# Kernel optimization log

Hardware: AMD Instinct MI355X
Metric: run time of the kernel (lower is better)

Reference implementation:

```python
import jax, jax.numpy as jnp
import numpy as np

B, T, D, H, E = 2, 1024, 1024, 4096, 8


def setup_inputs() -> dict:
    key = jax.random.key(0)
    ks = jax.random.split(key, 6)
    x = jax.random.normal(ks[0], (B, T, D), dtype=jnp.float32)
    padding_mask = jnp.zeros((B, T), dtype=bool)
    # Gate: Linear(D, E, bias=False) -> weight (E, D)
    Wg = jax.random.normal(ks[1], (E, D), dtype=jnp.float32) * (1.0 / np.sqrt(D))
    # Stacked expert FFN params (torch Linear layout: weight (out, in))
    W1 = jax.random.normal(ks[2], (E, H, D), dtype=jnp.float32) * (1.0 / np.sqrt(D))
    b1 = jax.random.normal(ks[3], (E, H), dtype=jnp.float32) * 0.01
    W2 = jax.random.normal(ks[4], (E, D, H), dtype=jnp.float32) * (1.0 / np.sqrt(H))
    b2 = jax.random.normal(ks[5], (E, D), dtype=jnp.float32) * 0.01
    return {"x": x, "padding_mask": padding_mask, "Wg": Wg, "W1": W1, "b1": b1, "W2": W2, "b2": b2}


def _top2_gate(xt, pm, Wg):
    # xt: (nt, D) flattened tokens, pm: (nt,) bool padding mask
    nt, ec = xt.shape[0], Wg.shape[0]
    logits = (xt @ Wg.T).astype(jnp.float32)            # use_fp32=True
    gate_value = jax.nn.softmax(logits, axis=-1)        # (nt, E)
    gate_value = jnp.where(pm[:, None], 0.0, gate_value)
    top2_idx = jax.lax.top_k(gate_value, 2)[1]          # (nt, 2)
    keep = jax.nn.one_hot(top2_idx, ec, dtype=bool).any(axis=1)  # (nt, E) True at top1/top2
    gate_weights = jnp.where(keep, gate_value, 0.0)
    s = gate_weights.sum(axis=1, keepdims=True)
    s = jnp.where(s == 0.0, 1.0, s)
    gate_weights = gate_weights / s
    # load-balance loss: fraction of top-1 assignments vs mean gate prob per expert
    nt_real = (~pm).sum().astype(jnp.float32)
    top1_counts = (jax.nn.one_hot(top2_idx[:, 0], ec, dtype=jnp.float32)
                   * (~pm)[:, None].astype(jnp.float32)).sum(axis=0)  # (E,)
    lb_loss = ec * ((top1_counts / nt_real) * (gate_value.sum(axis=0) / nt_real)).sum()
    return lb_loss, gate_weights, gate_value


def reference(x, padding_mask, Wg, W1, b1, W2, b2):
    Bx, Tx, Dx = x.shape
    xt = x.reshape(-1, Dx)                   # (nt, D)
    pm = padding_mask.reshape(-1)            # (nt,)
    lb_loss, gw, gate_value = _top2_gate(xt, pm, Wg)
    gw = gw.astype(x.dtype)                  # (nt, E)
    # Expert FFNs (dense over experts; routing weights are zero except top-2)
    h = jax.nn.relu(jnp.einsum('nd,ehd->neh', xt, W1) + b1)   # (nt, E, H)
    y = jnp.einsum('neh,edh->ned', h, W2) + b2                # (nt, E, D)
    out = jnp.einsum('ne,ned->nd', gw, y).reshape(Bx, Tx, Dx)
    return out, gate_value, lb_loss
```

## Files before the change

### kernel.cpp

```cpp
#include <hip/hip_runtime.h>
#include <hip/hip_bf16.h>
#include <stdint.h>


#define NTOK 2048
#define DDIM 1024
#define HDIM 4096
#define NEXP 8
#define KSPLIT 4

typedef float  f32x4  __attribute__((ext_vector_type(4)));
typedef __bf16 bf16x8 __attribute__((ext_vector_type(8)));
typedef __bf16 bf16x4 __attribute__((ext_vector_type(4)));

typedef const __attribute__((address_space(1))) void g1_t;
typedef __attribute__((address_space(3))) void l3_t;
__device__ __forceinline__ void gld16(const void* g, void* l) {
  __builtin_amdgcn_global_load_lds((g1_t*)g, (l3_t*)l, 16, 0, 0);
}

__global__ void init_kernel(int* fill) {
  int t = threadIdx.x;
  if (t < NEXP) fill[t] = 0;
}

__global__ __launch_bounds__(256)
void conv_kernel(const float* __restrict__ src, __bf16* __restrict__ dst, long n8) {
  long i = (long)blockIdx.x * 256 + threadIdx.x;
  long stride = (long)gridDim.x * 256;
  for (; i < n8; i += stride) {
    f32x4 a = ((const f32x4*)src)[2 * i];
    f32x4 b = ((const f32x4*)src)[2 * i + 1];
    bf16x8 o;
#pragma unroll
    for (int q = 0; q < 4; ++q) { o[q] = (__bf16)a[q]; o[q + 4] = (__bf16)b[q]; }
    ((bf16x8*)dst)[i] = o;
  }
}

__global__ __launch_bounds__(256)
void zero_y_kernel(float* __restrict__ y) {
  size_t i = (size_t)blockIdx.x * 256 + threadIdx.x;
  ((f32x4*)y)[i] = (f32x4){0.f, 0.f, 0.f, 0.f};
}

__global__ __launch_bounds__(256)
void gate_kernel(const float* __restrict__ x, const unsigned char* __restrict__ pmask,
                 const float* __restrict__ Wg, float* __restrict__ gate_out,
                 int* __restrict__ tix, float* __restrict__ twt,
                 __bf16* __restrict__ xbf)
{
  int wave = threadIdx.x >> 6, lane = threadIdx.x & 63;
  int t = blockIdx.x * 4 + wave;
  const f32x4* x4 = (const f32x4*)(x + (size_t)t * DDIM);
  const f32x4* w4 = (const f32x4*)Wg;
  bf16x4* xb4 = (bf16x4*)(xbf + (size_t)t * DDIM);
  float acc[NEXP];
#pragma unroll
  for (int e = 0; e < NEXP; ++e) acc[e] = 0.f;
#pragma unroll
  for (int i = 0; i < 4; ++i) {
    f32x4 xv = x4[i * 64 + lane];
    bf16x4 xo;
#pragma unroll
    for (int q = 0; q < 4; ++q) xo[q] = (__bf16)xv[q];
    xb4[i * 64 + lane] = xo;
#pragma unroll
    for (int e = 0; e < NEXP; ++e) {
      f32x4 wv = w4[e * 256 + i * 64 + lane];
      acc[e] += xv[0]*wv[0] + xv[1]*wv[1] + xv[2]*wv[2] + xv[3]*wv[3];
    }
  }
#pragma unroll
  for (int e = 0; e < NEXP; ++e) {
    float v = acc[e];
#pragma unroll
    for (int off = 32; off > 0; off >>= 1) v += __shfl_xor(v, off, 64);
    acc[e] = v;
  }
  if (lane == 0) {
    bool pm = pmask[t] != 0;
    float m = acc[0];
#pragma unroll
    for (int e = 1; e < NEXP; ++e) m = fmaxf(m, acc[e]);
    float g[NEXP]; float s = 0.f;
#pragma unroll
    for (int e = 0; e < NEXP; ++e) { g[e] = expf(acc[e] - m); s += g[e]; }
    float inv = 1.f / s;
#pragma unroll
    for (int e = 0; e < NEXP; ++e) g[e] *= inv;
    if (pm) {
#pragma unroll
      for (int e = 0; e < NEXP; ++e) g[e] = 0.f;
    }
    int i1 = 0;
#pragma unroll
    for (int e = 1; e < NEXP; ++e) if (g[e] > g[i1]) i1 = e;
    int i2 = -1;
#pragma unroll
    for (int e = 0; e < NEXP; ++e) if (e != i1 && (i2 < 0 || g[e] > g[i2])) i2 = e;
    float w1 = g[i1], w2 = g[i2], ss = w1 + w2;
    if (ss == 0.f) ss = 1.f;
    w1 /= ss; w2 /= ss;
#pragma unroll
    for (int e = 0; e < NEXP; ++e) gate_out[(size_t)t * NEXP + e] = g[e];
    tix[2*t] = i1; tix[2*t+1] = i2;
    twt[2*t] = w1; twt[2*t+1] = w2;
  }
}

__global__ __launch_bounds__(1024)
void stats_kernel(const float* __restrict__ gate_out, const int* __restrict__ tix,
                  const unsigned char* __restrict__ pmask,
                  int* __restrict__ ecount, int* __restrict__ offs,
                  float* __restrict__ lb_out)
{
  int tid = threadIdx.x, lane = tid & 63, wv = tid >> 6;
  float lg[NEXP]; float lt1[NEXP]; int lec[NEXP]; float ln = 0.f;
#pragma unroll
  for (int e = 0; e < NEXP; ++e) { lg[e] = 0.f; lt1[e] = 0.f; lec[e] = 0; }
#pragma unroll
  for (int it = 0; it < NTOK / 1024; ++it) {
    int t = tid + it * 1024;
    f32x4 g0 = ((const f32x4*)(gate_out + (size_t)t * NEXP))[0];
    f32x4 g1 = ((const f32x4*)(gate_out + (size_t)t * NEXP))[1];
    lg[0] += g0[0]; lg[1] += g0[1]; lg[2] += g0[2]; lg[3] += g0[3];
    lg[4] += g1[0]; lg[5] += g1[1]; lg[6] += g1[2]; lg[7] += g1[3];
    if (!pmask[t]) {
      int i1 = tix[2*t], i2 = tix[2*t+1];
      lt1[i1] += 1.f; lec[i1] += 1; lec[i2] += 1; ln += 1.f;
    }
  }
#pragma unroll
  for (int e = 0; e < NEXP; ++e) {
#pragma unroll
    for (int off = 32; off > 0; off >>= 1) {
      lg[e]  += __shfl_xor(lg[e],  off, 64);
      lt1[e] += __shfl_xor(lt1[e], off, 64);
      lec[e] += __shfl_xor(lec[e], off, 64);
    }
  }
#pragma unroll
  for (int off = 32; off > 0; off >>= 1) ln += __shfl_xor(ln, off, 64);
  __shared__ float sg[16][NEXP], st[16][NEXP], sn[16];
  __shared__ int   se[16][NEXP];
  if (lane == 0) {
#pragma unroll
    for (int e = 0; e < NEXP; ++e) { sg[wv][e] = lg[e]; st[wv][e] = lt1[e]; se[wv][e] = lec[e]; }
    sn[wv] = ln;
  }
  __syncthreads();
  if (tid == 0) {
    float G[NEXP] = {0}, T1[NEXP] = {0}; int EC[NEXP] = {0}; float N = 0.f;
    for (int w = 0; w < 16; ++w) {
      N += sn[w];
#pragma unroll
      for (int e = 0; e < NEXP; ++e) { G[e] += sg[w][e]; T1[e] += st[w][e]; EC[e] += se[w][e]; }
    }
    int o = 0;
    for (int e = 0; e < NEXP; ++e) { ecount[e] = EC[e]; offs[e] = o; o += EC[e]; }
    if (N <= 0.f) N = 1.f;
    float lb = 0.f;
    for (int e = 0; e < NEXP; ++e) lb += (T1[e] / N) * (G[e] / N);
    lb_out[0] = (float)NEXP * lb;
  }
}

__global__ __launch_bounds__(256)
void compact_kernel(const unsigned char* __restrict__ pmask, const int* __restrict__ tix,
                    const int* __restrict__ offs, int* __restrict__ fill,
                    int* __restrict__ tok_list, int* __restrict__ slot_of)
{
  int t = blockIdx.x * 256 + threadIdx.x;
  int lane = threadIdx.x & 63;
  bool pm = pmask[t] != 0;
#pragma unroll
  for (int j = 0; j < 2; ++j) {
    int e = pm ? -1 : tix[2*t + j];
    int pos = -1;
#pragma unroll
    for (int ex = 0; ex < NEXP; ++ex) {
      unsigned long long mask = __ballot(e == ex);
      if (mask) {
        int leader = (int)(__ffsll((long long)mask) - 1);
        int base = 0;
        if (lane == leader) base = atomicAdd(&fill[ex], (int)__popcll(mask));
        base = __shfl(base, leader, 64);
        if (e == ex)
          pos = offs[ex] + base + (int)__popcll(mask & ((1ull << lane) - 1ull));
      }
    }
    if (e >= 0) { tok_list[pos] = t; slot_of[2*t + j] = pos; }
    else slot_of[2*t + j] = -1;
  }
}

__global__ __launch_bounds__(256)
void gemm1_kernel(const __bf16* __restrict__ xbf, const __bf16* __restrict__ w1bf,
                  const float* __restrict__ b1, const int* __restrict__ ecount,
                  const int* __restrict__ offs, const int* __restrict__ tok_list,
                  __bf16* __restrict__ hbuf)
{
  const int NTILE = HDIM / 128;
  const int MTILE = NTOK / 128;
  int bid = blockIdx.x;
  int e = bid / (MTILE * NTILE);
  int rem = bid % (MTILE * NTILE);
  int mt = rem / NTILE, nt = rem % NTILE;
  int cnt = ecount[e];
  if (mt * 128 >= cnt) return;
  int off = offs[e];

  __shared__ __bf16 At[128 * 64];
  __shared__ __bf16 Bt[128 * 64];

  int tid = threadIdx.x, lane = tid & 63, wave = tid >> 6;
  int wm = wave >> 1, wn = wave & 1;

  const __bf16* aP[4];
  const __bf16* bP[4];
#pragma unroll
  for (int r = 0; r < 4; ++r) {
    int row = r * 32 + wave * 8 + (lane >> 3);
    int mrow = mt * 128 + row;
    int tok = tok_list[off + ((mrow < cnt) ? mrow : 0)];
    aP[r] = xbf + (size_t)tok * DDIM + (lane & 7) * 8;
    bP[r] = w1bf + (size_t)e * HDIM * DDIM + (size_t)(nt * 128 + row) * DDIM + (lane & 7) * 8;
  }
  __bf16* lA = At + wave * 512;
  __bf16* lB = Bt + wave * 512;

  f32x4 acc[4][4];
#pragma unroll
  for (int m = 0; m < 4; ++m)
#pragma unroll
    for (int n = 0; n < 4; ++n) acc[m][n] = (f32x4){0.f, 0.f, 0.f, 0.f};

  for (int k0 = 0; k0 < DDIM; k0 += 64) {
#pragma unroll
    for (int r = 0; r < 4; ++r) {
      gld16(aP[r] + k0, lA + r * 2048);
      gld16(bP[r] + k0, lB + r * 2048);
    }
    __syncthreads();
#pragma unroll
    for (int ks = 0; ks < 2; ++ks) {
      int koff = ks * 32 + (lane >> 4) * 8;
      bf16x8 af[4], bfr[4];
#pragma unroll
      for (int m = 0; m < 4; ++m) af[m] = *(const bf16x8*)&At[(wm*64 + m*16 + (lane & 15)) * 64 + koff];
#pragma unroll
      for (int n = 0; n < 4; ++n) bfr[n] = *(const bf16x8*)&Bt[(wn*64 + n*16 + (lane & 15)) * 64 + koff];
#pragma unroll
      for (int m = 0; m < 4; ++m)
#pragma unroll
        for (int n = 0; n < 4; ++n)
          acc[m][n] = __builtin_amdgcn_mfma_f32_16x16x32_bf16(af[m], bfr[n], acc[m][n], 0, 0, 0);
    }
    __syncthreads();
  }
#pragma unroll
  for (int n = 0; n < 4; ++n) {
    int col = nt * 128 + wn * 64 + n * 16 + (lane & 15);
    float bias = b1[e * HDIM + col];
#pragma unroll
    for (int m = 0; m < 4; ++m) {
#pragma unroll
      for (int j = 0; j < 4; ++j) {
        int mr = mt * 128 + wm * 64 + m * 16 + ((lane >> 4) << 2) + j;
        if (mr < cnt) {
          float v = fmaxf(acc[m][n][j] + bias, 0.f);
          hbuf[(size_t)(off + mr) * HDIM + col] = (__bf16)v;
        }
      }
    }
  }
}

__global__ __launch_bounds__(256)
void gemm2_kernel(const __bf16* __restrict__ hbuf, const __bf16* __restrict__ w2bf,
                  const int* __restrict__ ecount, const int* __restrict__ offs,
                  float* __restrict__ ybuf)
{
  const int NTILE = DDIM / 128;
  const int MTILE = NTOK / 128;
  int bid = blockIdx.x;
  int e = bid / (MTILE * NTILE * KSPLIT);
  int rem = bid % (MTILE * NTILE * KSPLIT);
  int mt = rem / (NTILE * KSPLIT);
  int rem2 = rem % (NTILE * KSPLIT);
  int nt = rem2 / KSPLIT, kc = rem2 % KSPLIT;
  int cnt = ecount[e];
  if (mt * 128 >= cnt) return;
  int off = offs[e];

  __shared__ __bf16 At[128 * 64];
  __shared__ __bf16 Bt[128 * 64];

  int tid = threadIdx.x, lane = tid & 63, wave = tid >> 6;
  int wm = wave >> 1, wn = wave & 1;

  const __bf16* aP[4];
  const __bf16* bP[4];
#pragma unroll
  for (int r = 0; r < 4; ++r) {
    int row = r * 32 + wave * 8 + (lane >> 3);
    aP[r] = hbuf + (size_t)(off + mt * 128 + row) * HDIM + (lane & 7) * 8;
    bP[r] = w2bf + (size_t)e * DDIM * HDIM + (size_t)(nt * 128 + row) * HDIM + (lane & 7) * 8;
  }
  __bf16* lA = At + wave * 512;
  __bf16* lB = Bt + wave * 512;

  f32x4 acc[4][4];
#pragma unroll
  for (int m = 0; m < 4; ++m)
#pragma unroll
    for (int n = 0; n < 4; ++n) acc[m][n] = (f32x4){0.f, 0.f, 0.f, 0.f};

  int kbeg = kc * (HDIM / KSPLIT);
  int kend = kbeg + (HDIM / KSPLIT);
  for (int k0 = kbeg; k0 < kend; k0 += 64) {
#pragma unroll
    for (int r = 0; r < 4; ++r) {
      gld16(aP[r] + k0, lA + r * 2048);
      gld16(bP[r] + k0, lB + r * 2048);
    }
    __syncthreads();
#pragma unroll
    for (int ks = 0; ks < 2; ++ks) {
      int koff = ks * 32 + (lane >> 4) * 8;
      bf16x8 af[4], bfr[4];
#pragma unroll
      for (int m = 0; m < 4; ++m) af[m] = *(const bf16x8*)&At[(wm*64 + m*16 + (lane & 15)) * 64 + koff];
#pragma unroll
      for (int n = 0; n < 4; ++n) bfr[n] = *(const bf16x8*)&Bt[(wn*64 + n*16 + (lane & 15)) * 64 + koff];
#pragma unroll
      for (int m = 0; m < 4; ++m)
#pragma unroll
        for (int n = 0; n < 4; ++n)
          acc[m][n] = __builtin_amdgcn_mfma_f32_16x16x32_bf16(af[m], bfr[n], acc[m][n], 0, 0, 0);
    }
    __syncthreads();
  }
#pragma unroll
  for (int m = 0; m < 4; ++m) {
#pragma unroll
    for (int j = 0; j < 4; ++j) {
      int mr = mt * 128 + wm * 64 + m * 16 + ((lane >> 4) << 2) + j;
      if (mr >= cnt) continue;
      int slot = off + mr;
#pragma unroll
      for (int n = 0; n < 4; ++n) {
        int col = nt * 128 + wn * 64 + n * 16 + (lane & 15);
        atomicAdd(&ybuf[(size_t)slot * DDIM + col], acc[m][n][j]);
      }
    }
  }
}

__global__ __launch_bounds__(256)
void combine_kernel(const float* __restrict__ ybuf, const int* __restrict__ slot_of,
                    const int* __restrict__ tix, const float* __restrict__ twt,
                    const float* __restrict__ b2, float* __restrict__ out)
{
  int t = blockIdx.x;
  int d4 = threadIdx.x;
  int sA = slot_of[2*t], sB = slot_of[2*t + 1];
  f32x4 r = (f32x4){0.f, 0.f, 0.f, 0.f};
  if (sA >= 0) {
    float wA = twt[2*t];
    f32x4 y = ((const f32x4*)(ybuf + (size_t)sA * DDIM))[d4];
    f32x4 b = ((const f32x4*)(b2 + (size_t)tix[2*t] * DDIM))[d4];
    r += wA * (y + b);
  }
  if (sB >= 0) {
    float wB = twt[2*t + 1];
    f32x4 y = ((const f32x4*)(ybuf + (size_t)sB * DDIM))[d4];
    f32x4 b = ((const f32x4*)(b2 + (size_t)tix[2*t + 1] * DDIM))[d4];
    r += wB * (y + b);
  }
  ((f32x4*)(out + (size_t)t * DDIM))[d4] = r;
}

extern "C" void kernel_launch(void* const* d_in, const int* in_sizes, int n_in,
                              void* d_out, int out_size, void* d_ws, size_t ws_size,
                              hipStream_t stream)
{
  const float* x  = (const float*)d_in[0];
  const unsigned char* pm = (const unsigned char*)d_in[1];
  const float* Wg = (const float*)d_in[2];
  const float* W1 = (const float*)d_in[3];
  const float* b1 = (const float*)d_in[4];
  const float* W2 = (const float*)d_in[5];
  const float* b2 = (const float*)d_in[6];
  float* out = (float*)d_out;
  float* gate_out = out + (size_t)NTOK * DDIM;
  float* lb_out = gate_out + (size_t)NTOK * NEXP;

  char* w = (char*)d_ws;
  int*   ecount   = (int*)(w + 0);
  int*   offs     = (int*)(w + 64);
  int*   fill     = (int*)(w + 128);
  int*   tix      = (int*)(w + 512);
  float* twt      = (float*)(w + 512 + 16384);
  int*   tok_list = (int*)(w + 512 + 32768);
  int*   slot_of  = (int*)(w + 512 + 49152);
  uintptr_t p = ((uintptr_t)(w + 512 + 65536) + 255) & ~(uintptr_t)255;
  __bf16* xbf  = (__bf16*)p;
  p += (size_t)NTOK * DDIM * 2;
  __bf16* wbf  = (__bf16*)p;
  p += (size_t)NEXP * HDIM * DDIM * 2;
  __bf16* hbuf = (__bf16*)p;
  p += (size_t)(2 * NTOK + 128) * HDIM * 2;
  float*  ybuf = (float*)p;

  init_kernel<<<1, 64, 0, stream>>>(fill);
  conv_kernel<<<2048, 256, 0, stream>>>(W1, wbf, (long)NEXP * HDIM * DDIM / 8);
  zero_y_kernel<<<(2 * NTOK * DDIM / 4) / 256, 256, 0, stream>>>(ybuf);
  gate_kernel<<<NTOK / 4, 256, 0, stream>>>(x, pm, Wg, gate_out, tix, twt, xbf);
  stats_kernel<<<1, 1024, 0, stream>>>(gate_out, tix, pm, ecount, offs, lb_out);
  compact_kernel<<<NTOK / 256, 256, 0, stream>>>(pm, tix, offs, fill, tok_list, slot_of);
  gemm1_kernel<<<NEXP * (NTOK / 128) * (HDIM / 128), 256, 0, stream>>>(xbf, wbf, b1, ecount, offs, tok_list, hbuf);
  conv_kernel<<<2048, 256, 0, stream>>>(W2, wbf, (long)NEXP * DDIM * HDIM / 8);
  gemm2_kernel<<<NEXP * (NTOK / 128) * (DDIM / 128) * KSPLIT, 256, 0, stream>>>(hbuf, wbf, ecount, offs, ybuf);
  combine_kernel<<<NTOK, 256, 0, stream>>>(ybuf, slot_of, tix, twt, b2, out);
}
```

Before: 300.6 us.

## Double-buffer LDS tiles with XOR swizzle in expert GEMMs, halve K-split

Both expert GEMM kernels now use two LDS buffers with a K-step of 32, issuing the next tile's global-to-LDS loads before computing on the current one, so memory latency overlaps with MFMA work. The LDS layout gains an XOR swizzle on the 16-byte chunk index to cut bank conflicts on fragment reads. GEMM2's K-split drops from 4 to 2, which halves the atomic adds into the output buffer but also halves the block count. The risks are less parallelism in GEMM2 and a single barrier per iteration that now guards buffer reuse across iterations.

```diff
diff --git a/kernel.cpp b/kernel.cpp
--- a/kernel.cpp
+++ b/kernel.cpp
@@ -7,7 +7,7 @@
 #define DDIM 1024
 #define HDIM 4096
 #define NEXP 8
-#define KSPLIT 4
+#define KSPLIT 2
 
 typedef float  f32x4  __attribute__((ext_vector_type(4)));
 typedef __bf16 bf16x8 __attribute__((ext_vector_type(8)));
@@ -195,6 +195,7 @@
   }
 }
 
+
 __global__ __launch_bounds__(256)
 void gemm1_kernel(const __bf16* __restrict__ xbf, const __bf16* __restrict__ w1bf,
                   const float* __restrict__ b1, const int* __restrict__ ecount,
@@ -211,24 +212,24 @@
   if (mt * 128 >= cnt) return;
   int off = offs[e];
 
-  __shared__ __bf16 At[128 * 64];
-  __shared__ __bf16 Bt[128 * 64];
+  __shared__ __bf16 As[2][128 * 32];
+  __shared__ __bf16 Bs[2][128 * 32];
 
   int tid = threadIdx.x, lane = tid & 63, wave = tid >> 6;
   int wm = wave >> 1, wn = wave & 1;
 
-  const __bf16* aP[4];
-  const __bf16* bP[4];
-#pragma unroll
-  for (int r = 0; r < 4; ++r) {
-    int row = r * 32 + wave * 8 + (lane >> 3);
+  const __bf16* aP[2];
+  const __bf16* bP[2];
+#pragma unroll
+  for (int c = 0; c < 2; ++c) {
+    int row = c * 64 + (tid >> 2);
+    int cd = (tid & 3) ^ ((row >> 1) & 3);
     int mrow = mt * 128 + row;
     int tok = tok_list[off + ((mrow < cnt) ? mrow : 0)];
-    aP[r] = xbf + (size_t)tok * DDIM + (lane & 7) * 8;
-    bP[r] = w1bf + (size_t)e * HDIM * DDIM + (size_t)(nt * 128 + row) * DDIM + (lane & 7) * 8;
-  }
-  __bf16* lA = At + wave * 512;
-  __bf16* lB = Bt + wave * 512;
+    aP[c] = xbf + (size_t)tok * DDIM + cd * 8;
+    bP[c] = w1bf + (size_t)e * HDIM * DDIM + (size_t)(nt * 128 + row) * DDIM + cd * 8;
+  }
+  int cg = ((lane >> 4) ^ ((lane >> 1) & 3)) << 3;
 
   f32x4 acc[4][4];
 #pragma unroll
@@ -236,29 +237,37 @@
 #pragma unroll
     for (int n = 0; n < 4; ++n) acc[m][n] = (f32x4){0.f, 0.f, 0.f, 0.f};
 
-  for (int k0 = 0; k0 < DDIM; k0 += 64) {
-#pragma unroll
-    for (int r = 0; r < 4; ++r) {
-      gld16(aP[r] + k0, lA + r * 2048);
-      gld16(bP[r] + k0, lB + r * 2048);
-    }
+  const int NIT = DDIM / 32;
+#pragma unroll
+  for (int c = 0; c < 2; ++c) {
+    gld16(aP[c], &As[0][(c * 64 + wave * 16) * 32]);
+    gld16(bP[c], &Bs[0][(c * 64 + wave * 16) * 32]);
+  }
+  __syncthreads();
+
+  for (int it = 0; it < NIT; ++it) {
+    int cur = it & 1;
+    if (it + 1 < NIT) {
+      int k0 = (it + 1) * 32;
+#pragma unroll
+      for (int c = 0; c < 2; ++c) {
+        gld16(aP[c] + k0, &As[cur ^ 1][(c * 64 + wave * 16) * 32]);
+        gld16(bP[c] + k0, &Bs[cur ^ 1][(c * 64 + wave * 16) * 32]);
+      }
+    }
+    bf16x8 af[4], bfr[4];
+#pragma unroll
+    for (int m = 0; m < 4; ++m) af[m]  = *(const bf16x8*)&As[cur][(wm*64 + m*16 + (lane & 15)) * 32 + cg];
+#pragma unroll
+    for (int n = 0; n < 4; ++n) bfr[n] = *(const bf16x8*)&Bs[cur][(wn*64 + n*16 + (lane & 15)) * 32 + cg];
+#pragma unroll
+    for (int m = 0; m < 4; ++m)
+#pragma unroll
+      for (int n = 0; n < 4; ++n)
+        acc[m][n] = __builtin_amdgcn_mfma_f32_16x16x32_bf16(af[m], bfr[n], acc[m][n], 0, 0, 0);
     __syncthreads();
-#pragma unroll
-    for (int ks = 0; ks < 2; ++ks) {
-      int koff = ks * 32 + (lane >> 4) * 8;
-      bf16x8 af[4], bfr[4];
-#pragma unroll
-      for (int m = 0; m < 4; ++m) af[m] = *(const bf16x8*)&At[(wm*64 + m*16 + (lane & 15)) * 64 + koff];
-#pragma unroll
-      for (int n = 0; n < 4; ++n) bfr[n] = *(const bf16x8*)&Bt[(wn*64 + n*16 + (lane & 15)) * 64 + koff];
-#pragma unroll
-      for (int m = 0; m < 4; ++m)
-#pragma unroll
-        for (int n = 0; n < 4; ++n)
-          acc[m][n] = __builtin_amdgcn_mfma_f32_16x16x32_bf16(af[m], bfr[n], acc[m][n], 0, 0, 0);
-    }
-    __syncthreads();
-  }
+  }
+
 #pragma unroll
   for (int n = 0; n < 4; ++n) {
     int col = nt * 128 + wn * 64 + n * 16 + (lane & 15);
@@ -294,22 +303,22 @@
   if (mt * 128 >= cnt) return;
   int off = offs[e];
 
-  __shared__ __bf16 At[128 * 64];
-  __shared__ __bf16 Bt[128 * 64];
+  __shared__ __bf16 As[2][128 * 32];
+  __shared__ __bf16 Bs[2][128 * 32];
 
   int tid = threadIdx.x, lane = tid & 63, wave = tid >> 6;
   int wm = wave >> 1, wn = wave & 1;
 
-  const __bf16* aP[4];
-  const __bf16* bP[4];
-#pragma unroll
-  for (int r = 0; r < 4; ++r) {
-    int row = r * 32 + wave * 8 + (lane >> 3);
-    aP[r] = hbuf + (size_t)(off + mt * 128 + row) * HDIM + (lane & 7) * 8;
-    bP[r] = w2bf + (size_t)e * DDIM * HDIM + (size_t)(nt * 128 + row) * HDIM + (lane & 7) * 8;
-  }
-  __bf16* lA = At + wave * 512;
-  __bf16* lB = Bt + wave * 512;
+  const __bf16* aP[2];
+  const __bf16* bP[2];
+#pragma unroll
+  for (int c = 0; c < 2; ++c) {
+    int row = c * 64 + (tid >> 2);
+    int cd = (tid & 3) ^ ((row >> 1) & 3);
+    aP[c] = hbuf + (size_t)(off + mt * 128 + row) * HDIM + cd * 8;
+    bP[c] = w2bf + (size_t)e * DDIM * HDIM + (size_t)(nt * 128 + row) * HDIM + cd * 8;
+  }
+  int cg = ((lane >> 4) ^ ((lane >> 1) & 3)) << 3;
 
   f32x4 acc[4][4];
 #pragma unroll
@@ -317,31 +326,39 @@
 #pragma unroll
     for (int n = 0; n < 4; ++n) acc[m][n] = (f32x4){0.f, 0.f, 0.f, 0.f};
 
-  int kbeg = kc * (HDIM / KSPLIT);
-  int kend = kbeg + (HDIM / KSPLIT);
-  for (int k0 = kbeg; k0 < kend; k0 += 64) {
-#pragma unroll
-    for (int r = 0; r < 4; ++r) {
-      gld16(aP[r] + k0, lA + r * 2048);
-      gld16(bP[r] + k0, lB + r * 2048);
-    }
+  const int KCH = HDIM / KSPLIT;
+  const int NIT = KCH / 32;
+  int kbeg = kc * KCH;
+#pragma unroll
+  for (int c = 0; c < 2; ++c) {
+    gld16(aP[c] + kbeg, &As[0][(c * 64 + wave * 16) * 32]);
+    gld16(bP[c] + kbeg, &Bs[0][(c * 64 + wave * 16) * 32]);
+  }
+  __syncthreads();
+
+  for (int it = 0; it < NIT; ++it) {
+    int cur = it & 1;
+    if (it + 1 < NIT) {
+      int k0 = kbeg + (it + 1) * 32;
+#pragma unroll
+      for (int c = 0; c < 2; ++c) {
+        gld16(aP[c] + k0, &As[cur ^ 1][(c * 64 + wave * 16) * 32]);
+        gld16(bP[c] + k0, &Bs[cur ^ 1][(c * 64 + wave * 16) * 32]);
+      }
+    }
+    bf16x8 af[4], bfr[4];
+#pragma unroll
+    for (int m = 0; m < 4; ++m) af[m]  = *(const bf16x8*)&As[cur][(wm*64 + m*16 + (lane & 15)) * 32 + cg];
+#pragma unroll
+    for (int n = 0; n < 4; ++n) bfr[n] = *(const bf16x8*)&Bs[cur][(wn*64 + n*16 + (lane & 15)) * 32 + cg];
+#pragma unroll
+    for (int m = 0; m < 4; ++m)
+#pragma unroll
+      for (int n = 0; n < 4; ++n)
+        acc[m][n] = __builtin_amdgcn_mfma_f32_16x16x32_bf16(af[m], bfr[n], acc[m][n], 0, 0, 0);
     __syncthreads();
-#pragma unroll
-    for (int ks = 0; ks < 2; ++ks) {
-      int koff = ks * 32 + (lane >> 4) * 8;
-      bf16x8 af[4], bfr[4];
-#pragma unroll
-      for (int m = 0; m < 4; ++m) af[m] = *(const bf16x8*)&At[(wm*64 + m*16 + (lane & 15)) * 64 + koff];
-#pragma unroll
-      for (int n = 0; n < 4; ++n) bfr[n] = *(const bf16x8*)&Bt[(wn*64 + n*16 + (lane & 15)) * 64 + koff];
-#pragma unroll
-      for (int m = 0; m < 4; ++m)
-#pragma unroll
-        for (int n = 0; n < 4; ++n)
-          acc[m][n] = __builtin_amdgcn_mfma_f32_16x16x32_bf16(af[m], bfr[n], acc[m][n], 0, 0, 0);
-    }
-    __syncthreads();
-  }
+  }
+
 #pragma unroll
   for (int m = 0; m < 4; ++m) {
 #pragma unroll
```

Result: faster. 267.3 us (-11.1%).
